# Optimization experiments

Measured on AMD Instinct MI355X. Metric: run time of the kernel, lower is better.

Reference implementation:

```python
import jax, jax.numpy as jnp
import numpy as np

N = 100000      # total nodes
E = 800000      # directed edges
DIN = 256       # input feature dim
H = 128         # hidden dim
EPS = 1e-5      # BatchNorm eps


def setup_inputs() -> dict:
    key = jax.random.key(0)
    ks = jax.random.split(key, 18)
    s = 0.05
    return {
        "x": jax.random.normal(ks[0], (N, DIN), jnp.float32),
        "src": jax.random.randint(ks[1], (E,), 0, N, dtype=jnp.int32),
        "dst": jax.random.randint(ks[2], (E,), 0, N, dtype=jnp.int32),
        "W1": jax.random.normal(ks[3], (DIN, H), jnp.float32) * s,
        "b1": jnp.zeros((H,), jnp.float32),
        "g1": jnp.ones((H,), jnp.float32),
        "be1": jnp.zeros((H,), jnp.float32),
        "W2": jax.random.normal(ks[4], (H, H), jnp.float32) * s,
        "b2": jnp.zeros((H,), jnp.float32),
        "g2": jnp.ones((H,), jnp.float32),
        "be2": jnp.zeros((H,), jnp.float32),
        "W3": jax.random.normal(ks[5], (H, H), jnp.float32) * s,
        "b3": jnp.zeros((H,), jnp.float32),
        "g3": jnp.ones((H,), jnp.float32),
        "be3": jnp.zeros((H,), jnp.float32),
        "Wf": jax.random.normal(ks[6], (H, 1), jnp.float32) * s,
        "bf": jnp.zeros((1,), jnp.float32),
    }


def _gcn_conv(h, W, b, src, dst, dis):
    # GCNConv: project, then sym-normalized aggregation over edges + self-loops
    h = h @ W                                   # [N, out]
    coef = dis[src] * dis[dst]                  # [E] edge norm weights
    agg = jax.ops.segment_sum(h[src] * coef[:, None], dst, num_segments=N)
    agg = agg + h * (dis * dis)[:, None]        # self-loop term (norm = 1/deg)
    return agg + b


def _bn_relu(h, g, be):
    # BatchNorm1d in training mode (batch stats over nodes, biased variance)
    mu = jnp.mean(h, axis=0)
    var = jnp.var(h, axis=0)
    return jax.nn.relu((h - mu) * (g / jnp.sqrt(var + EPS)) + be)


def reference(x, src, dst, W1, b1, g1, be1, W2, b2, g2, be2,
              W3, b3, g3, be3, Wf, bf):
    # degree of (A + I) counted on destination nodes, edge weight 1
    deg = jax.ops.segment_sum(jnp.ones((E,), jnp.float32), dst, num_segments=N) + 1.0
    dis = jax.lax.rsqrt(deg)                    # deg >= 1, safe

    h = _bn_relu(_gcn_conv(x, W1, b1, src, dst, dis), g1, be1)
    h = _bn_relu(_gcn_conv(h, W2, b2, src, dst, dis), g2, be2)
    h = _bn_relu(_gcn_conv(h, W3, b3, src, dst, dis), g3, be3)
    return h @ Wf + bf                          # [N, 1]
```

## Files before the change

### kernel.cpp

```cpp
#include <hip/hip_runtime.h>
#include <hip/hip_bf16.h>

typedef unsigned short ushort_t;
typedef __bf16 bf16x8 __attribute__((ext_vector_type(8)));
typedef unsigned short ushort8 __attribute__((ext_vector_type(8)));
typedef float f32x4 __attribute__((ext_vector_type(4)));

#define HH 128
#define EPS 1e-5f
#define STAT_SLICES 32

__device__ __forceinline__ float bf2f(ushort_t u) {
    unsigned v = ((unsigned)u) << 16;
    return __builtin_bit_cast(float, v);
}
__device__ __forceinline__ ushort_t f2bf(float f) {
    unsigned u = __builtin_bit_cast(unsigned, f);
    unsigned r = (u + 0x7fffu + ((u >> 16) & 1u)) >> 16;
    return (ushort_t)r;
}
__device__ __forceinline__ float cvt(const void* p, int i, int flag) {
    return flag ? bf2f(((const ushort_t*)p)[i]) : ((const float*)p)[i];
}

__global__ void setupK(const void* g1, const void* b1, const void* b2, const void* b3,
                       const void* g2, const void* g3,
                       const void* be1, const void* be2, const void* be3,
                       const void* Wf, const void* bfp,
                       float* __restrict__ cvec, int* __restrict__ flagp) {
    __shared__ int sflag;
    int t = threadIdx.x;
    if (t == 0) {
        int f = (((const ushort_t*)g1)[0] == 0x3F80) ? 1 : 0;
        sflag = f;
        flagp[0] = f;
    }
    __syncthreads();
    int f = sflag;
    cvec[t]         = cvt(b1, t, f);
    cvec[128 + t]   = cvt(b2, t, f);
    cvec[256 + t]   = cvt(b3, t, f);
    cvec[384 + t]   = cvt(g1, t, f);
    cvec[512 + t]   = cvt(g2, t, f);
    cvec[640 + t]   = cvt(g3, t, f);
    cvec[768 + t]   = cvt(be1, t, f);
    cvec[896 + t]   = cvt(be2, t, f);
    cvec[1024 + t]  = cvt(be3, t, f);
    cvec[1152 + t]  = cvt(Wf, t, f);
    if (t == 0) cvec[1280] = cvt(bfp, 0, f);
}

__global__ void histK(const int* __restrict__ dst, int* __restrict__ counts, int E) {
    int e = blockIdx.x * 256 + threadIdx.x;
    if (e < E) atomicAdd(&counts[dst[e]], 1);
}

__global__ void disK(const int* __restrict__ counts, float* __restrict__ dis, int n) {
    int i = blockIdx.x * 256 + threadIdx.x;
    if (i < n) dis[i] = rsqrtf((float)counts[i] + 1.0f);
}

__global__ void scanA(const int* __restrict__ cnt, int* __restrict__ partial, int n) {
    __shared__ int lds[256];
    int tid = threadIdx.x;
    int base = blockIdx.x * 2048 + tid * 8;
    int s = 0;
#pragma unroll
    for (int j = 0; j < 8; ++j) { int idx = base + j; if (idx < n) s += cnt[idx]; }
    lds[tid] = s; __syncthreads();
    for (int off = 128; off; off >>= 1) { if (tid < off) lds[tid] += lds[tid + off]; __syncthreads(); }
    if (tid == 0) partial[blockIdx.x] = lds[0];
}

__global__ void scanB(int* __restrict__ partial, int* __restrict__ rowptr, int nb, int n) {
    if (threadIdx.x == 0) {
        int running = 0;
        for (int i = 0; i < nb; ++i) { int v = partial[i]; partial[i] = running; running += v; }
        rowptr[n] = running;
    }
}

__global__ void scanC(const int* __restrict__ cnt, const int* __restrict__ partial,
                      int* __restrict__ rowptr, int n) {
    __shared__ int lds[256];
    int tid = threadIdx.x;
    int base = blockIdx.x * 2048 + tid * 8;
    int v[8]; int s = 0;
#pragma unroll
    for (int j = 0; j < 8; ++j) { int idx = base + j; v[j] = (idx < n) ? cnt[idx] : 0; s += v[j]; }
    lds[tid] = s; __syncthreads();
    for (int off = 1; off < 256; off <<= 1) {
        int x = (tid >= off) ? lds[tid - off] : 0;
        __syncthreads();
        lds[tid] += x;
        __syncthreads();
    }
    int excl = lds[tid] - s;
    int off0 = partial[blockIdx.x] + excl;
#pragma unroll
    for (int j = 0; j < 8; ++j) {
        int idx = base + j;
        if (idx < n) { rowptr[idx] = off0; off0 += v[j]; }
    }
}

__global__ void scatterK(const int* __restrict__ src, const int* __restrict__ dst,
                         const int* __restrict__ rowptr, int* __restrict__ fill,
                         const float* __restrict__ dis,
                         int* __restrict__ esrc, float* __restrict__ ecoef, int E) {
    int e = blockIdx.x * 256 + threadIdx.x;
    if (e >= E) return;
    int d = dst[e], s = src[e];
    int pos = rowptr[d] + atomicAdd(&fill[d], 1);
    esrc[pos] = s;
    ecoef[pos] = dis[s] * dis[d];
}

__global__ void trK(const void* __restrict__ W, ushort_t* __restrict__ Wt, int K, int Kp,
                    const int* __restrict__ flagp) {
    int idx = blockIdx.x * 256 + threadIdx.x;
    if (idx >= K * HH) return;
    int flag = flagp[0];
    int k = idx >> 7, n = idx & 127;
    ushort_t v = flag ? ((const ushort_t*)W)[idx] : f2bf(((const float*)W)[idx]);
    Wt[n * Kp + k] = v;
}

template <bool BN, bool EXT, int K>
__global__ __launch_bounds__(256) void mmK(const void* __restrict__ Av,
                                           const ushort_t* __restrict__ Wt,
                                           ushort_t* __restrict__ out,
                                           int n,
                                           const float* __restrict__ scale,
                                           const float* __restrict__ shift,
                                           const int* __restrict__ flagp) {
    constexpr int KP  = K + 8;
    constexpr int BKP = 136;
    constexpr int NCH = K / 128;
    constexpr int NST = K / 32;

    __shared__ ushort_t bs[128 * BKP];

    const int tid  = threadIdx.x;
    const int lane = tid & 63;
    const int wave = tid >> 6;
    const int m = lane & 15;
    const int q = lane >> 4;
    const int flag = EXT ? flagp[0] : 1;

    int rowA = blockIdx.x * 64 + wave * 16 + m;
    int rA = rowA < n ? rowA : (n - 1);

    ushort8 a[NST];
    if (EXT && !flag) {
        const float* ap32 = (const float*)Av + (size_t)rA * K + q * 8;
#pragma unroll
        for (int s = 0; s < NST; ++s) {
            float4 f0 = *(const float4*)(ap32 + s * 32);
            float4 f1 = *(const float4*)(ap32 + s * 32 + 4);
            a[s][0] = f2bf(f0.x); a[s][1] = f2bf(f0.y); a[s][2] = f2bf(f0.z); a[s][3] = f2bf(f0.w);
            a[s][4] = f2bf(f1.x); a[s][5] = f2bf(f1.y); a[s][6] = f2bf(f1.z); a[s][7] = f2bf(f1.w);
        }
    } else {
        const ushort_t* ap16 = (const ushort_t*)Av + (size_t)rA * K + q * 8;
#pragma unroll
        for (int s = 0; s < NST; ++s) a[s] = *(const ushort8*)(ap16 + s * 32);
    }
    if (BN) {
#pragma unroll
        for (int s = 0; s < NST; ++s) {
            int kb = s * 32 + q * 8;
#pragma unroll
            for (int j = 0; j < 8; ++j) {
                float f = fmaxf(bf2f(a[s][j]) * scale[kb + j] + shift[kb + j], 0.f);
                a[s][j] = f2bf(f);
            }
        }
    }

    f32x4 acc[8];
#pragma unroll
    for (int t = 0; t < 8; ++t) acc[t] = (f32x4){0.f, 0.f, 0.f, 0.f};

#pragma unroll
    for (int c = 0; c < NCH; ++c) {
#pragma unroll
        for (int r = 0; r < 8; ++r) {
            int idx = tid + r * 256;
            int row = idx >> 4, seg = idx & 15;
            *(uint4*)&bs[row * BKP + seg * 8] =
                *(const uint4*)&Wt[(size_t)row * KP + c * 128 + seg * 8];
        }
        __syncthreads();
#pragma unroll
        for (int s = 0; s < 4; ++s) {
            bf16x8 af = __builtin_bit_cast(bf16x8, a[c * 4 + s]);
#pragma unroll
            for (int t = 0; t < 8; ++t) {
                ushort8 bv = *(const ushort8*)&bs[(t * 16 + m) * BKP + s * 32 + q * 8];
                acc[t] = __builtin_amdgcn_mfma_f32_16x16x32_bf16(
                    af, __builtin_bit_cast(bf16x8, bv), acc[t], 0, 0, 0);
            }
        }
        if (c + 1 < NCH) __syncthreads();
    }

    const int rb = blockIdx.x * 64 + wave * 16 + q * 4;
#pragma unroll
    for (int t = 0; t < 8; ++t) {
#pragma unroll
        for (int r = 0; r < 4; ++r) {
            int rr = rb + r;
            if (rr < n) out[(size_t)rr * HH + t * 16 + m] = f2bf(acc[t][r]);
        }
    }
}

__global__ __launch_bounds__(256) void aggK(const ushort_t* __restrict__ t,
                                            const int* __restrict__ esrc,
                                            const float* __restrict__ ecoef,
                                            const int* __restrict__ rowptr,
                                            const float* __restrict__ dis,
                                            const float* __restrict__ bias,
                                            ushort_t* __restrict__ g,
                                            float* __restrict__ ssum, float* __restrict__ ssq,
                                            int n) {
    const int lane = threadIdx.x & 63;
    const int wave = threadIdx.x >> 6;
    const int cb = lane * 2;
    const float b0 = bias[cb], b1 = bias[cb + 1];
    float s0 = 0.f, s1 = 0.f, q0 = 0.f, q1 = 0.f;

    for (int node = blockIdx.x * 4 + wave; node < n; node += gridDim.x * 4) {
        float d = dis[node];
        float d2 = d * d;
        unsigned sv = *(const unsigned*)(t + (size_t)node * HH + cb);
        float a0 = bf2f((ushort_t)(sv & 0xffff)) * d2;
        float a1 = bf2f((ushort_t)(sv >> 16)) * d2;

        int beg = rowptr[node], end = rowptr[node + 1];
        for (int eb = beg; eb < end; eb += 64) {
            int rem = end - eb; if (rem > 64) rem = 64;
            int es = (lane < rem) ? esrc[eb + lane] : 0;
            float ec = (lane < rem) ? ecoef[eb + lane] : 0.f;
            int rr = (rem + 3) & ~3;
            for (int j = 0; j < rr; j += 4) {
                int i0 = __shfl(es, j),     i1 = __shfl(es, j + 1);
                int i2 = __shfl(es, j + 2), i3 = __shfl(es, j + 3);
                float c0 = __shfl(ec, j),     c1 = __shfl(ec, j + 1);
                float c2 = __shfl(ec, j + 2), c3 = __shfl(ec, j + 3);
                unsigned w0 = *(const unsigned*)(t + (size_t)i0 * HH + cb);
                unsigned w1 = *(const unsigned*)(t + (size_t)i1 * HH + cb);
                unsigned w2 = *(const unsigned*)(t + (size_t)i2 * HH + cb);
                unsigned w3 = *(const unsigned*)(t + (size_t)i3 * HH + cb);
                a0 += bf2f((ushort_t)(w0 & 0xffff)) * c0;
                a1 += bf2f((ushort_t)(w0 >> 16)) * c0;
                a0 += bf2f((ushort_t)(w1 & 0xffff)) * c1;
                a1 += bf2f((ushort_t)(w1 >> 16)) * c1;
                a0 += bf2f((ushort_t)(w2 & 0xffff)) * c2;
                a1 += bf2f((ushort_t)(w2 >> 16)) * c2;
                a0 += bf2f((ushort_t)(w3 & 0xffff)) * c3;
                a1 += bf2f((ushort_t)(w3 >> 16)) * c3;
            }
        }
        a0 += b0; a1 += b1;
        unsigned packed = (unsigned)f2bf(a0) | ((unsigned)f2bf(a1) << 16);
        *(unsigned*)(g + (size_t)node * HH + cb) = packed;
        s0 += a0; s1 += a1; q0 += a0 * a0; q1 += a1 * a1;
    }

    __shared__ float red[4][64][4];
    red[wave][lane][0] = s0; red[wave][lane][1] = s1;
    red[wave][lane][2] = q0; red[wave][lane][3] = q1;
    __syncthreads();
    if (wave == 0) {
        float S0 = 0, S1 = 0, Q0 = 0, Q1 = 0;
#pragma unroll
        for (int w = 0; w < 4; ++w) {
            S0 += red[w][lane][0]; S1 += red[w][lane][1];
            Q0 += red[w][lane][2]; Q1 += red[w][lane][3];
        }
        int slice = (blockIdx.x & (STAT_SLICES - 1)) * HH;
        atomicAdd(&ssum[slice + cb], S0);
        atomicAdd(&ssum[slice + cb + 1], S1);
        atomicAdd(&ssq[slice + cb], Q0);
        atomicAdd(&ssq[slice + cb + 1], Q1);
    }
}

__global__ void finK(const float* __restrict__ ssum, const float* __restrict__ ssq,
                     const float* __restrict__ gam, const float* __restrict__ bet,
                     float* __restrict__ scale, float* __restrict__ shift, int n) {
    int c = threadIdx.x;
    float S = 0.f, Q = 0.f;
    for (int sl = 0; sl < STAT_SLICES; ++sl) { S += ssum[sl * HH + c]; Q += ssq[sl * HH + c]; }
    float invn = 1.0f / (float)n;
    float mu = S * invn;
    float var = Q * invn - mu * mu;
    var = fmaxf(var, 0.f);
    float sc = gam[c] * rsqrtf(var + EPS);
    scale[c] = sc;
    shift[c] = bet[c] - mu * sc;
}

__global__ __launch_bounds__(256) void outK(const ushort_t* __restrict__ g,
                                            const float* __restrict__ scale,
                                            const float* __restrict__ shift,
                                            const float* __restrict__ Wf,
                                            const float* __restrict__ bfp,
                                            void* __restrict__ outv, int n,
                                            const int* __restrict__ flagp) {
    const int lane = threadIdx.x & 63;
    const int wave = threadIdx.x >> 6;
    const int cb = lane * 2;
    const float w0 = Wf[cb], w1 = Wf[cb + 1];
    const float sc0 = scale[cb], sc1 = scale[cb + 1];
    const float sh0 = shift[cb], sh1 = shift[cb + 1];
    const float bb = bfp[0];
    const int flag = flagp[0];

    for (int node = blockIdx.x * 4 + wave; node < n; node += gridDim.x * 4) {
        unsigned v = *(const unsigned*)(g + (size_t)node * HH + cb);
        float h0 = fmaxf(bf2f((ushort_t)(v & 0xffff)) * sc0 + sh0, 0.f);
        float h1 = fmaxf(bf2f((ushort_t)(v >> 16)) * sc1 + sh1, 0.f);
        float x = h0 * w0 + h1 * w1;
#pragma unroll
        for (int off = 32; off; off >>= 1) x += __shfl_down(x, off);
        if (lane == 0) {
            float r = x + bb;
            if (flag) ((ushort_t*)outv)[node] = f2bf(r);
            else      ((float*)outv)[node] = r;
        }
    }
}

extern "C" void kernel_launch(void* const* d_in, const int* in_sizes, int n_in,
                              void* d_out, int out_size, void* d_ws, size_t ws_size,
                              hipStream_t stream) {
    const int DIN = 256;
    const int N = in_sizes[0] / DIN;
    const int E = in_sizes[1];

    const void* x   = d_in[0];
    const int*  src = (const int*)d_in[1];
    const int*  dst = (const int*)d_in[2];
    const void* W1  = d_in[3];
    const void* b1  = d_in[4];
    const void* g1  = d_in[5];
    const void* be1 = d_in[6];
    const void* W2  = d_in[7];
    const void* b2  = d_in[8];
    const void* g2  = d_in[9];
    const void* be2 = d_in[10];
    const void* W3  = d_in[11];
    const void* b3  = d_in[12];
    const void* g3  = d_in[13];
    const void* be3 = d_in[14];
    const void* Wf  = d_in[15];
    const void* bfp = d_in[16];

    char* base = (char*)d_ws;
    size_t off = 0;
    auto carve = [&](size_t bytes) -> void* {
        void* p = base + off;
        off += (bytes + 255) & ~(size_t)255;
        return p;
    };
    int*      counts = (int*)carve((size_t)N * 4);
    float*    dis    = (float*)carve((size_t)N * 4);
    int*      rowptr = (int*)carve((size_t)(N + 1) * 4);
    int*      partial= (int*)carve(256 * 4);
    int*      esrc   = (int*)carve((size_t)E * 4);
    float*    ecoef  = (float*)carve((size_t)E * 4);
    ushort_t* Wt1    = (ushort_t*)carve((size_t)128 * 264 * 2);
    ushort_t* Wt2    = (ushort_t*)carve((size_t)128 * 136 * 2);
    ushort_t* Wt3    = (ushort_t*)carve((size_t)128 * 136 * 2);
    ushort_t* tbuf   = (ushort_t*)carve((size_t)N * HH * 2);
    ushort_t* gbuf   = (ushort_t*)carve((size_t)N * HH * 2);
    float*    stats  = (float*)carve((size_t)3 * 2 * STAT_SLICES * HH * 4);
    float*    scsh   = (float*)carve((size_t)3 * 2 * HH * 4);
    float*    cvec   = (float*)carve((size_t)1281 * 4);
    int*      flagp  = (int*)carve(256);

    float* ssum0 = stats;                         float* ssq0 = ssum0 + STAT_SLICES * HH;
    float* ssum1 = ssq0 + STAT_SLICES * HH;       float* ssq1 = ssum1 + STAT_SLICES * HH;
    float* ssum2 = ssq1 + STAT_SLICES * HH;       float* ssq2 = ssum2 + STAT_SLICES * HH;
    float* scale0 = scsh;            float* shift0 = scale0 + HH;
    float* scale1 = shift0 + HH;     float* shift1 = scale1 + HH;
    float* scale2 = shift1 + HH;     float* shift2 = scale2 + HH;

    float* c_b1 = cvec;         float* c_b2 = cvec + 128;  float* c_b3 = cvec + 256;
    float* c_g1 = cvec + 384;   float* c_g2 = cvec + 512;  float* c_g3 = cvec + 640;
    float* c_be1 = cvec + 768;  float* c_be2 = cvec + 896; float* c_be3 = cvec + 1024;
    float* c_Wf = cvec + 1152;  float* c_bf = cvec + 1280;

    const int nb = (N + 2047) / 2048;

    hipMemsetAsync(counts, 0, (size_t)N * 4, stream);
    hipMemsetAsync(stats, 0, (size_t)3 * 2 * STAT_SLICES * HH * 4, stream);

    setupK<<<1, 128, 0, stream>>>(g1, b1, b2, b3, g2, g3, be1, be2, be3, Wf, bfp, cvec, flagp);

    histK<<<(E + 255) / 256, 256, 0, stream>>>(dst, counts, E);
    disK<<<(N + 255) / 256, 256, 0, stream>>>(counts, dis, N);
    scanA<<<nb, 256, 0, stream>>>(counts, partial, N);
    scanB<<<1, 64, 0, stream>>>(partial, rowptr, nb, N);
    scanC<<<nb, 256, 0, stream>>>(counts, partial, rowptr, N);
    hipMemsetAsync(counts, 0, (size_t)N * 4, stream);
    scatterK<<<(E + 255) / 256, 256, 0, stream>>>(src, dst, rowptr, counts, dis, esrc, ecoef, E);

    trK<<<(DIN * HH + 255) / 256, 256, 0, stream>>>(W1, Wt1, DIN, DIN + 8, flagp);
    trK<<<(HH * HH + 255) / 256, 256, 0, stream>>>(W2, Wt2, HH, HH + 8, flagp);
    trK<<<(HH * HH + 255) / 256, 256, 0, stream>>>(W3, Wt3, HH, HH + 8, flagp);

    const int mmBlocks = (N + 63) / 64;
    const int aggBlocks = 4096;

    mmK<false, true, 256><<<mmBlocks, 256, 0, stream>>>(x, Wt1, tbuf, N, nullptr, nullptr, flagp);
    aggK<<<aggBlocks, 256, 0, stream>>>(tbuf, esrc, ecoef, rowptr, dis, c_b1, gbuf, ssum0, ssq0, N);
    finK<<<1, 128, 0, stream>>>(ssum0, ssq0, c_g1, c_be1, scale0, shift0, N);
    mmK<true, false, 128><<<mmBlocks, 256, 0, stream>>>(gbuf, Wt2, tbuf, N, scale0, shift0, flagp);
    aggK<<<aggBlocks, 256, 0, stream>>>(tbuf, esrc, ecoef, rowptr, dis, c_b2, gbuf, ssum1, ssq1, N);
    finK<<<1, 128, 0, stream>>>(ssum1, ssq1, c_g2, c_be2, scale1, shift1, N);
    mmK<true, false, 128><<<mmBlocks, 256, 0, stream>>>(gbuf, Wt3, tbuf, N, scale1, shift1, flagp);
    aggK<<<aggBlocks, 256, 0, stream>>>(tbuf, esrc, ecoef, rowptr, dis, c_b3, gbuf, ssum2, ssq2, N);
    finK<<<1, 128, 0, stream>>>(ssum2, ssq2, c_g3, c_be3, scale2, shift2, N);
    outK<<<1024, 256, 0, stream>>>(gbuf, scale2, shift2, c_Wf, c_bf, d_out, N, flagp);
}
```

Baseline: 492.9 us.

## Pack edge records, unroll gather by 8, merge transposes and memsets

Edge source index and coefficient are interleaved into one 8-byte record, so each lane of the aggregation kernel issues a single load. The gather loop is unrolled to eight outstanding row loads for more memory-level parallelism. The scatter now counts down from the histogram counts with atomicSub, which drops the second memset, and the three weight transposes become one launch. Counts and stats are placed next to each other so a single memset clears both. Padding the gather to multiples of 8 adds wasted shuffles and loads of row 0 for low-degree nodes.

```diff
diff --git a/kernel.cpp b/kernel.cpp
--- a/kernel.cpp
+++ b/kernel.cpp
@@ -107,20 +107,28 @@
 __global__ void scatterK(const int* __restrict__ src, const int* __restrict__ dst,
                          const int* __restrict__ rowptr, int* __restrict__ fill,
                          const float* __restrict__ dis,
-                         int* __restrict__ esrc, float* __restrict__ ecoef, int E) {
+                         uint2* __restrict__ erec, int E) {
     int e = blockIdx.x * 256 + threadIdx.x;
     if (e >= E) return;
     int d = dst[e], s = src[e];
-    int pos = rowptr[d] + atomicAdd(&fill[d], 1);
-    esrc[pos] = s;
-    ecoef[pos] = dis[s] * dis[d];
-}
-
-__global__ void trK(const void* __restrict__ W, ushort_t* __restrict__ Wt, int K, int Kp,
+    int old = atomicSub(&fill[d], 1);
+    int pos = rowptr[d] + old - 1;
+    float c = dis[s] * dis[d];
+    uint2 r; r.x = (unsigned)s; r.y = __builtin_bit_cast(unsigned, c);
+    erec[pos] = r;
+}
+
+__global__ void trK(const void* __restrict__ W1, ushort_t* __restrict__ Wt1,
+                    const void* __restrict__ W2, ushort_t* __restrict__ Wt2,
+                    const void* __restrict__ W3, ushort_t* __restrict__ Wt3,
                     const int* __restrict__ flagp) {
     int idx = blockIdx.x * 256 + threadIdx.x;
-    if (idx >= K * HH) return;
     int flag = flagp[0];
+    const void* W; ushort_t* Wt; int Kp;
+    if (idx < 32768)       { W = W1; Wt = Wt1; Kp = 264; }
+    else if (idx < 49152)  { W = W2; Wt = Wt2; Kp = 136; idx -= 32768; }
+    else if (idx < 65536)  { W = W3; Wt = Wt3; Kp = 136; idx -= 49152; }
+    else return;
     int k = idx >> 7, n = idx & 127;
     ushort_t v = flag ? ((const ushort_t*)W)[idx] : f2bf(((const float*)W)[idx]);
     Wt[n * Kp + k] = v;
@@ -217,8 +225,7 @@
 }
 
 __global__ __launch_bounds__(256) void aggK(const ushort_t* __restrict__ t,
-                                            const int* __restrict__ esrc,
-                                            const float* __restrict__ ecoef,
+                                            const uint2* __restrict__ erec,
                                             const int* __restrict__ rowptr,
                                             const float* __restrict__ dis,
                                             const float* __restrict__ bias,
@@ -241,26 +248,25 @@
         int beg = rowptr[node], end = rowptr[node + 1];
         for (int eb = beg; eb < end; eb += 64) {
             int rem = end - eb; if (rem > 64) rem = 64;
-            int es = (lane < rem) ? esrc[eb + lane] : 0;
-            float ec = (lane < rem) ? ecoef[eb + lane] : 0.f;
-            int rr = (rem + 3) & ~3;
-            for (int j = 0; j < rr; j += 4) {
-                int i0 = __shfl(es, j),     i1 = __shfl(es, j + 1);
-                int i2 = __shfl(es, j + 2), i3 = __shfl(es, j + 3);
-                float c0 = __shfl(ec, j),     c1 = __shfl(ec, j + 1);
-                float c2 = __shfl(ec, j + 2), c3 = __shfl(ec, j + 3);
-                unsigned w0 = *(const unsigned*)(t + (size_t)i0 * HH + cb);
-                unsigned w1 = *(const unsigned*)(t + (size_t)i1 * HH + cb);
-                unsigned w2 = *(const unsigned*)(t + (size_t)i2 * HH + cb);
-                unsigned w3 = *(const unsigned*)(t + (size_t)i3 * HH + cb);
-                a0 += bf2f((ushort_t)(w0 & 0xffff)) * c0;
-                a1 += bf2f((ushort_t)(w0 >> 16)) * c0;
-                a0 += bf2f((ushort_t)(w1 & 0xffff)) * c1;
-                a1 += bf2f((ushort_t)(w1 >> 16)) * c1;
-                a0 += bf2f((ushort_t)(w2 & 0xffff)) * c2;
-                a1 += bf2f((ushort_t)(w2 >> 16)) * c2;
-                a0 += bf2f((ushort_t)(w3 & 0xffff)) * c3;
-                a1 += bf2f((ushort_t)(w3 >> 16)) * c3;
+            uint2 rec = (lane < rem) ? erec[eb + lane] : (uint2){0u, 0u};
+            int es = (int)rec.x;
+            float ec = __builtin_bit_cast(float, rec.y);
+            int rr = (rem + 7) & ~7;
+            for (int j = 0; j < rr; j += 8) {
+                int   ii[8]; float cc[8]; unsigned ww[8];
+#pragma unroll
+                for (int k = 0; k < 8; ++k) {
+                    ii[k] = __shfl(es, j + k);
+                    cc[k] = __shfl(ec, j + k);
+                }
+#pragma unroll
+                for (int k = 0; k < 8; ++k)
+                    ww[k] = *(const unsigned*)(t + (size_t)ii[k] * HH + cb);
+#pragma unroll
+                for (int k = 0; k < 8; ++k) {
+                    a0 += bf2f((ushort_t)(ww[k] & 0xffff)) * cc[k];
+                    a1 += bf2f((ushort_t)(ww[k] >> 16)) * cc[k];
+                }
             }
         }
         a0 += b0; a1 += b1;
@@ -367,27 +373,30 @@
         return p;
     };
     int*      counts = (int*)carve((size_t)N * 4);
+    float*    stats  = (float*)carve((size_t)3 * 2 * STAT_SLICES * HH * 4);
+    size_t    zbytes = off;
     float*    dis    = (float*)carve((size_t)N * 4);
     int*      rowptr = (int*)carve((size_t)(N + 1) * 4);
     int*      partial= (int*)carve(256 * 4);
-    int*      esrc   = (int*)carve((size_t)E * 4);
-    float*    ecoef  = (float*)carve((size_t)E * 4);
+    uint2*    erec   = (uint2*)carve((size_t)E * 8);
     ushort_t* Wt1    = (ushort_t*)carve((size_t)128 * 264 * 2);
     ushort_t* Wt2    = (ushort_t*)carve((size_t)128 * 136 * 2);
     ushort_t* Wt3    = (ushort_t*)carve((size_t)128 * 136 * 2);
     ushort_t* tbuf   = (ushort_t*)carve((size_t)N * HH * 2);
     ushort_t* gbuf   = (ushort_t*)carve((size_t)N * HH * 2);
-    float*    stats  = (float*)carve((size_t)3 * 2 * STAT_SLICES * HH * 4);
-    float*    scsh   = (float*)carve((size_t)3 * 2 * HH * 4);
     float*    cvec   = (float*)carve((size_t)1281 * 4);
     int*      flagp  = (int*)carve(256);
 
     float* ssum0 = stats;                         float* ssq0 = ssum0 + STAT_SLICES * HH;
     float* ssum1 = ssq0 + STAT_SLICES * HH;       float* ssq1 = ssum1 + STAT_SLICES * HH;
     float* ssum2 = ssq1 + STAT_SLICES * HH;       float* ssq2 = ssum2 + STAT_SLICES * HH;
-    float* scale0 = scsh;            float* shift0 = scale0 + HH;
+
+    float* scsh = cvec + 1344;
+    float* scshbuf = (float*)carve((size_t)3 * 2 * HH * 4);
+    float* scale0 = scshbuf;         float* shift0 = scale0 + HH;
     float* scale1 = shift0 + HH;     float* shift1 = scale1 + HH;
     float* scale2 = shift1 + HH;     float* shift2 = scale2 + HH;
+    (void)scsh;
 
     float* c_b1 = cvec;         float* c_b2 = cvec + 128;  float* c_b3 = cvec + 256;
     float* c_g1 = cvec + 384;   float* c_g2 = cvec + 512;  float* c_g3 = cvec + 640;
@@ -396,8 +405,7 @@
 
     const int nb = (N + 2047) / 2048;
 
-    hipMemsetAsync(counts, 0, (size_t)N * 4, stream);
-    hipMemsetAsync(stats, 0, (size_t)3 * 2 * STAT_SLICES * HH * 4, stream);
+    hipMemsetAsync(d_ws, 0, zbytes, stream);
 
     setupK<<<1, 128, 0, stream>>>(g1, b1, b2, b3, g2, g3, be1, be2, be3, Wf, bfp, cvec, flagp);
 
@@ -406,24 +414,21 @@
     scanA<<<nb, 256, 0, stream>>>(counts, partial, N);
     scanB<<<1, 64, 0, stream>>>(partial, rowptr, nb, N);
     scanC<<<nb, 256, 0, stream>>>(counts, partial, rowptr, N);
-    hipMemsetAsync(counts, 0, (size_t)N * 4, stream);
-    scatterK<<<(E + 255) / 256, 256, 0, stream>>>(src, dst, rowptr, counts, dis, esrc, ecoef, E);
-
-    trK<<<(DIN * HH + 255) / 256, 256, 0, stream>>>(W1, Wt1, DIN, DIN + 8, flagp);
-    trK<<<(HH * HH + 255) / 256, 256, 0, stream>>>(W2, Wt2, HH, HH + 8, flagp);
-    trK<<<(HH * HH + 255) / 256, 256, 0, stream>>>(W3, Wt3, HH, HH + 8, flagp);
+    scatterK<<<(E + 255) / 256, 256, 0, stream>>>(src, dst, rowptr, counts, dis, erec, E);
+
+    trK<<<256, 256, 0, stream>>>(W1, Wt1, W2, Wt2, W3, Wt3, flagp);
 
     const int mmBlocks = (N + 63) / 64;
     const int aggBlocks = 4096;
 
     mmK<false, true, 256><<<mmBlocks, 256, 0, stream>>>(x, Wt1, tbuf, N, nullptr, nullptr, flagp);
-    aggK<<<aggBlocks, 256, 0, stream>>>(tbuf, esrc, ecoef, rowptr, dis, c_b1, gbuf, ssum0, ssq0, N);
+    aggK<<<aggBlocks, 256, 0, stream>>>(tbuf, erec, rowptr, dis, c_b1, gbuf, ssum0, ssq0, N);
     finK<<<1, 128, 0, stream>>>(ssum0, ssq0, c_g1, c_be1, scale0, shift0, N);
     mmK<true, false, 128><<<mmBlocks, 256, 0, stream>>>(gbuf, Wt2, tbuf, N, scale0, shift0, flagp);
-    aggK<<<aggBlocks, 256, 0, stream>>>(tbuf, esrc, ecoef, rowptr, dis, c_b2, gbuf, ssum1, ssq1, N);
+    aggK<<<aggBlocks, 256, 0, stream>>>(tbuf, erec, rowptr, dis, c_b2, gbuf, ssum1, ssq1, N);
     finK<<<1, 128, 0, stream>>>(ssum1, ssq1, c_g2, c_be2, scale1, shift1, N);
     mmK<true, false, 128><<<mmBlocks, 256, 0, stream>>>(gbuf, Wt3, tbuf, N, scale1, shift1, flagp);
-    aggK<<<aggBlocks, 256, 0, stream>>>(tbuf, esrc, ecoef, rowptr, dis, c_b3, gbuf, ssum2, ssq2, N);
+    aggK<<<aggBlocks, 256, 0, stream>>>(tbuf, erec, rowptr, dis, c_b3, gbuf, ssum2, ssq2, N);
     finK<<<1, 128, 0, stream>>>(ssum2, ssq2, c_g3, c_be3, scale2, shift2, N);
     outK<<<1024, 256, 0, stream>>>(gbuf, scale2, shift2, c_Wf, c_bf, d_out, N, flagp);
 }
```

Measured after the change: 474.7 us. 1.04x faster.
